# Kernel tuning notes

Measured on AMD Instinct MI355X. Metric: run time of the kernel, lower is better.

Reference implementation:

```python
import jax, jax.numpy as jnp
import numpy as np

SEQ_LEN, BATCH, TAGS = 512, 1024, 32
START_IDX, END_IDX = 30, 31
NEG = -10000.0


def setup_inputs() -> dict:
    key = jax.random.key(0)
    k1, k2 = jax.random.split(key)
    feats = jax.random.normal(k1, (SEQ_LEN, BATCH, TAGS), dtype=jnp.float32)
    mask = jnp.ones((SEQ_LEN, BATCH), dtype=jnp.float32)
    # xavier-normal-ish transition, then apply START/END constraints as in reset_parameters
    transition = jax.random.normal(k2, (TAGS, TAGS), dtype=jnp.float32) * (2.0 / (TAGS + TAGS)) ** 0.5
    transition = transition.at[START_IDX, :].set(NEG)
    transition = transition.at[:, END_IDX].set(NEG)
    return {"feats": feats, "mask": mask, "transition": transition}


def reference(feats, mask, transition):
    # feats: (T, N, M), mask: (T, N), transition: (M, M)
    batch_size, tag_size = feats.shape[1], feats.shape[2]
    alpha0 = jnp.full((batch_size, tag_size), NEG, dtype=feats.dtype)
    alpha0 = alpha0.at[:, START_IDX].set(0.0)

    def step(alpha, inp):
        feat_t, mask_t = inp  # (N, M), (N,)
        # score[n, j, i] = alpha[n, i] + transition[j, i] + feat[n, j]
        score = alpha[:, None, :] + transition[None, :, :] + feat_t[:, :, None]
        new_alpha = jax.nn.logsumexp(score, axis=-1)  # (N, M)
        m = mask_t[:, None]
        alpha = new_alpha * m + alpha * (1.0 - m)
        return alpha, None

    alpha, _ = jax.lax.scan(step, alpha0, (feats, mask))
    alpha = alpha + transition[END_IDX][None, :]
    return jax.nn.logsumexp(alpha, axis=-1)  # (N,)
```

## Files before the change

### kernel.cpp

```cpp
#include <hip/hip_runtime.h>


constexpr int SEQ = 512, BATCH = 1024, TAGS = 32;
constexpr int BPB = 8;
constexpr int CH = 8;
constexpr int NCH = (SEQ / 2) / CH;
constexpr int RINGN = 2;
constexpr int SSTRIDE = BPB * TAGS;
constexpr int FSLOT = CH * SSTRIDE;
constexpr int MSLOT = CH * BPB;

#define LOG2E 1.4426950408889634f
#define LN2   0.6931471805599453f

typedef __attribute__((ext_vector_type(8))) short short8;
typedef __attribute__((ext_vector_type(4))) float float4v;
union Frag8 { unsigned u[4]; short8 v; };

__device__ __forceinline__ unsigned pk_rn(float x, float y) {
  return __builtin_amdgcn_perm(__float_as_uint(y) + 0x8000u,
                               __float_as_uint(x) + 0x8000u, 0x07060302u);
}
__device__ __forceinline__ unsigned pk_tr(float x, float y) {
  return __builtin_amdgcn_perm(__float_as_uint(y), __float_as_uint(x), 0x07060302u);
}

template <bool FWD>
__device__ __forceinline__ void produce(
    const float* __restrict__ feats, const float* __restrict__ maskp,
    float* __restrict__ FFd, float* __restrict__ MMd,
    unsigned* __restrict__ FLGd, int b0, int lane) {
  const int bl = lane >> 3;
  const int tgd = (lane & 7) * 4;
  const size_t t0off = FWD ? 0 : (size_t)(SEQ - 1) * BATCH * TAGS;
  const float* gF = feats + t0off + (size_t)(b0 + bl) * TAGS + tgd;
  const float* gM = maskp + b0 + (lane & 7) + (FWD ? 0 : (size_t)(SEQ - 1) * BATCH);
  const ptrdiff_t fstep = FWD ? (ptrdiff_t)(BATCH * TAGS) : -(ptrdiff_t)(BATCH * TAGS);
  const ptrdiff_t mstep = FWD ? (ptrdiff_t)BATCH : -(ptrdiff_t)BATCH;
  const int wd = bl * 32 + (((lane & 7) ^ (bl & 7)) << 2);

  float4v SA[CH], SB[CH];
  float mA, mB;

#define LOADC(S, MV, c)                                                       \
  { _Pragma("unroll") for (int j = 0; j < CH; ++j)                            \
      S[j] = *(const float4v*)(gF + (ptrdiff_t)(CH * (c) + j) * fstep);       \
    MV = gM[(ptrdiff_t)(CH * (c) + (lane >> 3)) * mstep]; }

#define PROC(S, MV, c)                                                        \
  { float* fb = FFd + ((c) & (RINGN - 1)) * FSLOT;                            \
    float* mb = MMd + ((c) & (RINGN - 1)) * MSLOT;                            \
    const unsigned flag = (__ballot(MV != 0.0f) == ~0ull) ? 1u : 0u;          \
    _Pragma("unroll") for (int j = 0; j < CH; ++j) {                          \
      float4v e;                                                              \
      _Pragma("unroll") for (int i = 0; i < 4; ++i)                           \
        e[i] = __builtin_amdgcn_exp2f(S[j][i] * LOG2E);                       \
      *(float4v*)(fb + j * SSTRIDE + wd) = e;                                 \
    }                                                                         \
    mb[lane] = MV;                                                            \
    if (lane == 0) FLGd[(c) & (RINGN - 1)] = flag; }

  LOADC(SA, mA, 0)
  LOADC(SB, mB, 1)
  PROC(SA, mA, 0)
  asm volatile("s_waitcnt lgkmcnt(0)" ::: "memory");
  __builtin_amdgcn_s_barrier();
#pragma unroll 2
  for (int k = 0; k < NCH; ++k) {
    if ((k & 1) == 0) {
      if (k + 2 < NCH) LOADC(SA, mA, k + 2)
      if (k + 1 < NCH) PROC(SB, mB, k + 1)
    } else {
      if (k + 2 < NCH) LOADC(SB, mB, k + 2)
      if (k + 1 < NCH) PROC(SA, mA, k + 1)
    }
    asm volatile("s_waitcnt lgkmcnt(0)" ::: "memory");
    __builtin_amdgcn_s_barrier();
  }
  __syncthreads();
#undef LOADC
#undef PROC
}

template <bool FWD>
__device__ __forceinline__ void consume(
    const float* __restrict__ trans, float* __restrict__ out,
    const float* __restrict__ FFd, const float* __restrict__ MMd,
    const unsigned* __restrict__ FLGd,
    float* __restrict__ vbuf, float* __restrict__ c2buf, int b0, int lane) {
  const int s = lane & 15, q = lane >> 4;

  int sig[8];
#pragma unroll
  for (int i = 0; i < 8; ++i) sig[i] = (i < 4) ? (4 * q + i) : (16 + 4 * q + (i - 4));
  Frag8 e0, e1;
#pragma unroll
  for (int p = 0; p < 4; ++p) {
    if (FWD) {
      e0.u[p] = pk_rn(__builtin_amdgcn_exp2f(trans[s * TAGS + sig[2 * p]] * LOG2E),
                      __builtin_amdgcn_exp2f(trans[s * TAGS + sig[2 * p + 1]] * LOG2E));
      e1.u[p] = pk_rn(__builtin_amdgcn_exp2f(trans[(16 + s) * TAGS + sig[2 * p]] * LOG2E),
                      __builtin_amdgcn_exp2f(trans[(16 + s) * TAGS + sig[2 * p + 1]] * LOG2E));
    } else {
      e0.u[p] = pk_rn(__builtin_amdgcn_exp2f(trans[sig[2 * p] * TAGS + s] * LOG2E),
                      __builtin_amdgcn_exp2f(trans[sig[2 * p + 1] * TAGS + s] * LOG2E));
      e1.u[p] = pk_rn(__builtin_amdgcn_exp2f(trans[sig[2 * p] * TAGS + 16 + s] * LOG2E),
                      __builtin_amdgcn_exp2f(trans[sig[2 * p + 1] * TAGS + 16 + s] * LOG2E));
    }
  }

  float a[8];
#pragma unroll
  for (int i = 0; i < 8; ++i) {
    if (FWD) a[i] = (q == 3 && i == 6) ? 1.0f : 0.0f;
    else a[i] = __builtin_amdgcn_exp2f(
        trans[31 * TAGS + ((i < 4) ? (4 * q + i) : (16 + 4 * q + (i - 4)))] * LOG2E);
  }
  Frag8 Bf;
  Bf.u[0] = pk_tr(a[0], a[1]); Bf.u[1] = pk_tr(a[2], a[3]);
  Bf.u[2] = pk_tr(a[4], a[5]); Bf.u[3] = pk_tr(a[6], a[7]);
  float c2 = 0.f;
  const float4v zerov = {0.f, 0.f, 0.f, 0.f};

  const int off0 = s * 32 + ((q ^ (s & 7)) << 2);
  const int off1 = s * 32 + (((q + 4) ^ (s & 7)) << 2);

  float4v rA0, rA1, rB0, rB1;

  __builtin_amdgcn_s_barrier();
  __builtin_amdgcn_sched_barrier(0);
  rA0 = *(const float4v*)(FFd + 0 * SSTRIDE + off0);
  rA1 = *(const float4v*)(FFd + 0 * SSTRIDE + off1);
  rB0 = *(const float4v*)(FFd + 1 * SSTRIDE + off0);
  rB1 = *(const float4v*)(FFd + 1 * SSTRIDE + off1);

#define RENORM_A()                                                            \
  { float mx = fmaxf(fmaxf(fmaxf(a[0], a[1]), fmaxf(a[2], a[3])),             \
                     fmaxf(fmaxf(a[4], a[5]), fmaxf(a[6], a[7])));            \
    mx = fmaxf(mx, __shfl_xor(mx, 16, 64));                                   \
    mx = fmaxf(mx, __shfl_xor(mx, 32, 64));                                   \
    const int ex = (int)((__float_as_uint(mx) >> 23) & 0xFFu) - 127;          \
    const float scl = __uint_as_float((unsigned)(127 - ex) << 23);            \
    _Pragma("unroll") for (int i = 0; i < 8; ++i) a[i] *= scl;                \
    c2 += (float)ex; }

  for (int k = 0; k < NCH; ++k) {
    const float* fb = FFd + (k & (RINGN - 1)) * FSLOT;
    const float* mb = MMd + (k & (RINGN - 1)) * MSLOT;
    const unsigned fl = __builtin_amdgcn_readfirstlane(FLGd[k & (RINGN - 1)]);
    if (fl) {
#pragma unroll
      for (int j = 0; j < CH; ++j) {
        const float4v F0 = (j & 1) ? rB0 : rA0;
        const float4v F1 = (j & 1) ? rB1 : rA1;
        if (FWD) {
          const float4v D0 = __builtin_amdgcn_mfma_f32_16x16x32_bf16(e0.v, Bf.v, zerov, 0, 0, 0);
          const float4v D1 = __builtin_amdgcn_mfma_f32_16x16x32_bf16(e1.v, Bf.v, zerov, 0, 0, 0);
#pragma unroll
          for (int i = 0; i < 4; ++i) { a[i] = D0[i] * F0[i]; a[4 + i] = D1[i] * F1[i]; }
          if (j == CH - 1) RENORM_A()
          Bf.u[0] = pk_tr(a[0], a[1]); Bf.u[1] = pk_tr(a[2], a[3]);
          Bf.u[2] = pk_tr(a[4], a[5]); Bf.u[3] = pk_tr(a[6], a[7]);
        } else {
          float tb[8];
#pragma unroll
          for (int i = 0; i < 4; ++i) { tb[i] = a[i] * F0[i]; tb[4 + i] = a[4 + i] * F1[i]; }
          Frag8 Bp;
          Bp.u[0] = pk_tr(tb[0], tb[1]); Bp.u[1] = pk_tr(tb[2], tb[3]);
          Bp.u[2] = pk_tr(tb[4], tb[5]); Bp.u[3] = pk_tr(tb[6], tb[7]);
          const float4v D0 = __builtin_amdgcn_mfma_f32_16x16x32_bf16(e0.v, Bp.v, zerov, 0, 0, 0);
          const float4v D1 = __builtin_amdgcn_mfma_f32_16x16x32_bf16(e1.v, Bp.v, zerov, 0, 0, 0);
#pragma unroll
          for (int i = 0; i < 4; ++i) { a[i] = D0[i]; a[4 + i] = D1[i]; }
          if (j == CH - 1) RENORM_A()
        }
        if (j < CH - 2) {
          ((j & 1) ? rB0 : rA0) = *(const float4v*)(fb + (j + 2) * SSTRIDE + off0);
          ((j & 1) ? rB1 : rA1) = *(const float4v*)(fb + (j + 2) * SSTRIDE + off1);
        }
      }
    } else {
#pragma unroll
      for (int j = 0; j < CH; ++j) {
        const float4v F0 = (j & 1) ? rB0 : rA0;
        const float4v F1 = (j & 1) ? rB1 : rA1;
        const bool mv = (mb[j * BPB + (s & 7)] != 0.0f);
        if (FWD) {
          const float4v D0 = __builtin_amdgcn_mfma_f32_16x16x32_bf16(e0.v, Bf.v, zerov, 0, 0, 0);
          const float4v D1 = __builtin_amdgcn_mfma_f32_16x16x32_bf16(e1.v, Bf.v, zerov, 0, 0, 0);
#pragma unroll
          for (int i = 0; i < 4; ++i) {
            a[i] = mv ? D0[i] * F0[i] : a[i];
            a[4 + i] = mv ? D1[i] * F1[i] : a[4 + i];
          }
          if (j == CH - 1) RENORM_A()
          Bf.u[0] = pk_tr(a[0], a[1]); Bf.u[1] = pk_tr(a[2], a[3]);
          Bf.u[2] = pk_tr(a[4], a[5]); Bf.u[3] = pk_tr(a[6], a[7]);
        } else {
          float tb[8];
#pragma unroll
          for (int i = 0; i < 4; ++i) { tb[i] = a[i] * F0[i]; tb[4 + i] = a[4 + i] * F1[i]; }
          Frag8 Bp;
          Bp.u[0] = pk_tr(tb[0], tb[1]); Bp.u[1] = pk_tr(tb[2], tb[3]);
          Bp.u[2] = pk_tr(tb[4], tb[5]); Bp.u[3] = pk_tr(tb[6], tb[7]);
          const float4v D0 = __builtin_amdgcn_mfma_f32_16x16x32_bf16(e0.v, Bp.v, zerov, 0, 0, 0);
          const float4v D1 = __builtin_amdgcn_mfma_f32_16x16x32_bf16(e1.v, Bp.v, zerov, 0, 0, 0);
#pragma unroll
          for (int i = 0; i < 4; ++i) {
            a[i] = mv ? D0[i] : a[i];
            a[4 + i] = mv ? D1[i] : a[4 + i];
          }
          if (j == CH - 1) RENORM_A()
        }
        if (j < CH - 2) {
          ((j & 1) ? rB0 : rA0) = *(const float4v*)(fb + (j + 2) * SSTRIDE + off0);
          ((j & 1) ? rB1 : rA1) = *(const float4v*)(fb + (j + 2) * SSTRIDE + off1);
        }
      }
    }
    asm volatile("s_waitcnt lgkmcnt(0)" ::: "memory");
    __builtin_amdgcn_s_barrier();
    __builtin_amdgcn_sched_barrier(0);
    if (k < NCH - 1) {
      const float* fn = FFd + ((k + 1) & (RINGN - 1)) * FSLOT;
      rA0 = *(const float4v*)(fn + 0 * SSTRIDE + off0);
      rA1 = *(const float4v*)(fn + 0 * SSTRIDE + off1);
      rB0 = *(const float4v*)(fn + 1 * SSTRIDE + off0);
      rB1 = *(const float4v*)(fn + 1 * SSTRIDE + off1);
    }
  }
#undef RENORM_A

  if (!FWD) {
    float4v lo = {a[0], a[1], a[2], a[3]}, hi = {a[4], a[5], a[6], a[7]};
    *(float4v*)(vbuf + lane * 8) = lo;
    *(float4v*)(vbuf + lane * 8 + 4) = hi;
    if (lane < 8) c2buf[lane] = c2;
  }
  __syncthreads();
  if (FWD) {
    const float4v v0 = *(const float4v*)(vbuf + lane * 8);
    const float4v v1 = *(const float4v*)(vbuf + lane * 8 + 4);
    float dot = a[0] * v0[0] + a[1] * v0[1] + a[2] * v0[2] + a[3] * v0[3] +
                a[4] * v1[0] + a[5] * v1[1] + a[6] * v1[2] + a[7] * v1[3];
    dot += __shfl_xor(dot, 16, 64);
    dot += __shfl_xor(dot, 32, 64);
    if (lane < 8)
      out[b0 + lane] = LN2 * (c2 + c2buf[lane] + __builtin_amdgcn_logf(dot));
  }
}

extern "C" __global__ void __launch_bounds__(256, 1) crf_scan(
    const float* __restrict__ feats, const float* __restrict__ mask,
    const float* __restrict__ trans, float* __restrict__ out) {
  __shared__ float FF[2][RINGN][FSLOT];
  __shared__ float MM[2][RINGN][MSLOT];
  __shared__ unsigned FLG[2][RINGN];
  __shared__ float vbuf[512];
  __shared__ float c2buf[16];
  const int wid = threadIdx.x >> 6;
  const int lane = threadIdx.x & 63;
  const int b0 = blockIdx.x * BPB;

  if (wid == 0)
    consume<true>(trans, out, &FF[0][0][0], &MM[0][0][0], &FLG[0][0], vbuf, c2buf, b0, lane);
  else if (wid == 1)
    consume<false>(trans, out, &FF[1][0][0], &MM[1][0][0], &FLG[1][0], vbuf, c2buf, b0, lane);
  else if (wid == 2)
    produce<true>(feats, mask, &FF[0][0][0], &MM[0][0][0], &FLG[0][0], b0, lane);
  else
    produce<false>(feats, mask, &FF[1][0][0], &MM[1][0][0], &FLG[1][0], b0, lane);
}

extern "C" void kernel_launch(void* const* d_in, const int* in_sizes, int n_in,
                              void* d_out, int out_size, void* d_ws, size_t ws_size,
                              hipStream_t stream) {
  const float* feats = (const float*)d_in[0];
  const float* mask  = (const float*)d_in[1];
  const float* trans = (const float*)d_in[2];
  float* out = (float*)d_out;
  hipLaunchKernelGGL(crf_scan, dim3(BATCH / BPB), dim3(256), 0, stream,
                     feats, mask, trans, out);
}
```

Measured before the change: 106.9 us.

## Stream feats into LDS via async global_load_lds with four-deep raw ring

The producer wave now issues direct global-to-LDS loads into a four-slot raw ring instead of loading the chunks into registers. A separate transform pass reads the raw LDS data, applies exp2, and writes the double-buffered tile the consumer reads. This deepens the prefetch to four chunks ahead without register pressure, aiming to hide global memory latency in the serial scan. In exchange it uses more LDS, adds an extra LDS read per element, and depends on hand-counted vmcnt waits being correct.

```diff
diff --git a/kernel.cpp b/kernel.cpp
--- a/kernel.cpp
+++ b/kernel.cpp
@@ -5,9 +5,10 @@
 constexpr int BPB = 8;
 constexpr int CH = 8;
 constexpr int NCH = (SEQ / 2) / CH;
-constexpr int RINGN = 2;
+constexpr int RRN = 4;
 constexpr int SSTRIDE = BPB * TAGS;
 constexpr int FSLOT = CH * SSTRIDE;
+constexpr int RSLOT = FSLOT + 64;
 constexpr int MSLOT = CH * BPB;
 
 #define LOG2E 1.4426950408889634f
@@ -25,61 +26,76 @@
   return __builtin_amdgcn_perm(__float_as_uint(y), __float_as_uint(x), 0x07060302u);
 }
 
+__device__ __forceinline__ void gld16(const float* g, float* l) {
+  __builtin_amdgcn_global_load_lds((const __attribute__((address_space(1))) void*)g,
+                                   (__attribute__((address_space(3))) void*)l, 16, 0, 0);
+}
+__device__ __forceinline__ void gld4(const float* g, float* l) {
+  __builtin_amdgcn_global_load_lds((const __attribute__((address_space(1))) void*)g,
+                                   (__attribute__((address_space(3))) void*)l, 4, 0, 0);
+}
+
 template <bool FWD>
 __device__ __forceinline__ void produce(
     const float* __restrict__ feats, const float* __restrict__ maskp,
-    float* __restrict__ FFd, float* __restrict__ MMd,
+    float* __restrict__ RAWd, float* __restrict__ FFd, float* __restrict__ MMd,
     unsigned* __restrict__ FLGd, int b0, int lane) {
-  const int bl = lane >> 3;
-  const int tgd = (lane & 7) * 4;
+  const int bs = lane >> 3;
+  const int tg = 4 * ((lane & 7) ^ (bs & 7));
   const size_t t0off = FWD ? 0 : (size_t)(SEQ - 1) * BATCH * TAGS;
-  const float* gF = feats + t0off + (size_t)(b0 + bl) * TAGS + tgd;
-  const float* gM = maskp + b0 + (lane & 7) + (FWD ? 0 : (size_t)(SEQ - 1) * BATCH);
+  const float* gF0 = feats + t0off + (size_t)(b0 + bs) * TAGS + tg;
+  const float* gM0 = maskp +
+      (FWD ? (size_t)(lane >> 3) : (size_t)(SEQ - 1 - (lane >> 3))) * BATCH +
+      b0 + (lane & 7);
   const ptrdiff_t fstep = FWD ? (ptrdiff_t)(BATCH * TAGS) : -(ptrdiff_t)(BATCH * TAGS);
   const ptrdiff_t mstep = FWD ? (ptrdiff_t)BATCH : -(ptrdiff_t)BATCH;
-  const int wd = bl * 32 + (((lane & 7) ^ (bl & 7)) << 2);
-
-  float4v SA[CH], SB[CH];
-  float mA, mB;
-
-#define LOADC(S, MV, c)                                                       \
-  { _Pragma("unroll") for (int j = 0; j < CH; ++j)                            \
-      S[j] = *(const float4v*)(gF + (ptrdiff_t)(CH * (c) + j) * fstep);       \
-    MV = gM[(ptrdiff_t)(CH * (c) + (lane >> 3)) * mstep]; }
-
-#define PROC(S, MV, c)                                                        \
-  { float* fb = FFd + ((c) & (RINGN - 1)) * FSLOT;                            \
-    float* mb = MMd + ((c) & (RINGN - 1)) * MSLOT;                            \
-    const unsigned flag = (__ballot(MV != 0.0f) == ~0ull) ? 1u : 0u;          \
-    _Pragma("unroll") for (int j = 0; j < CH; ++j) {                          \
-      float4v e;                                                              \
-      _Pragma("unroll") for (int i = 0; i < 4; ++i)                           \
-        e[i] = __builtin_amdgcn_exp2f(S[j][i] * LOG2E);                       \
-      *(float4v*)(fb + j * SSTRIDE + wd) = e;                                 \
-    }                                                                         \
-    mb[lane] = MV;                                                            \
-    if (lane == 0) FLGd[(c) & (RINGN - 1)] = flag; }
-
-  LOADC(SA, mA, 0)
-  LOADC(SB, mB, 1)
-  PROC(SA, mA, 0)
+
+  auto FILL = [&](int k) {
+    float* rb = RAWd + (k & (RRN - 1)) * RSLOT;
+#pragma unroll
+    for (int j = 0; j < CH; ++j)
+      gld16(gF0 + (ptrdiff_t)(CH * k + j) * fstep, rb + j * SSTRIDE);
+    gld4(gM0 + (ptrdiff_t)(CH * k) * mstep, rb + FSLOT);
+  };
+
+  auto XFORM = [&](int c) {
+    const float* rb = RAWd + (c & (RRN - 1)) * RSLOT;
+    float* fb = FFd + (c & 1) * FSLOT;
+    const float mraw = rb[FSLOT + lane];
+    const unsigned flag = (__ballot(mraw != 0.0f) == ~0ull) ? 1u : 0u;
+#pragma unroll
+    for (int j = 0; j < CH; ++j) {
+      const float4v r = *(const float4v*)(rb + j * SSTRIDE + lane * 4);
+      float4v e;
+#pragma unroll
+      for (int i = 0; i < 4; ++i) e[i] = __builtin_amdgcn_exp2f(r[i] * LOG2E);
+      *(float4v*)(fb + j * SSTRIDE + lane * 4) = e;
+    }
+    MMd[(c & 1) * MSLOT + lane] = mraw;
+    if (lane == 0) FLGd[c & 1] = flag;
+  };
+
+  FILL(0); FILL(1); FILL(2); FILL(3);
+  asm volatile("s_waitcnt vmcnt(27)" ::: "memory");
+  XFORM(0);
   asm volatile("s_waitcnt lgkmcnt(0)" ::: "memory");
   __builtin_amdgcn_s_barrier();
-#pragma unroll 2
   for (int k = 0; k < NCH; ++k) {
-    if ((k & 1) == 0) {
-      if (k + 2 < NCH) LOADC(SA, mA, k + 2)
-      if (k + 1 < NCH) PROC(SB, mB, k + 1)
-    } else {
-      if (k + 2 < NCH) LOADC(SB, mB, k + 2)
-      if (k + 1 < NCH) PROC(SA, mA, k + 1)
-    }
+    if (k < NCH - 4) {
+      FILL(k + 4);
+      asm volatile("s_waitcnt vmcnt(27)" ::: "memory");
+    } else if (k == NCH - 4) {
+      asm volatile("s_waitcnt vmcnt(18)" ::: "memory");
+    } else if (k == NCH - 3) {
+      asm volatile("s_waitcnt vmcnt(9)" ::: "memory");
+    } else if (k == NCH - 2) {
+      asm volatile("s_waitcnt vmcnt(0)" ::: "memory");
+    }
+    if (k + 1 < NCH) XFORM(k + 1);
     asm volatile("s_waitcnt lgkmcnt(0)" ::: "memory");
     __builtin_amdgcn_s_barrier();
   }
   __syncthreads();
-#undef LOADC
-#undef PROC
 }
 
 template <bool FWD>
@@ -145,9 +161,9 @@
     c2 += (float)ex; }
 
   for (int k = 0; k < NCH; ++k) {
-    const float* fb = FFd + (k & (RINGN - 1)) * FSLOT;
-    const float* mb = MMd + (k & (RINGN - 1)) * MSLOT;
-    const unsigned fl = __builtin_amdgcn_readfirstlane(FLGd[k & (RINGN - 1)]);
+    const float* fb = FFd + (k & 1) * FSLOT;
+    const float* mb = MMd + (k & 1) * MSLOT;
+    const unsigned fl = __builtin_amdgcn_readfirstlane(FLGd[k & 1]);
     if (fl) {
 #pragma unroll
       for (int j = 0; j < CH; ++j) {
@@ -222,7 +238,7 @@
     __builtin_amdgcn_s_barrier();
     __builtin_amdgcn_sched_barrier(0);
     if (k < NCH - 1) {
-      const float* fn = FFd + ((k + 1) & (RINGN - 1)) * FSLOT;
+      const float* fn = FFd + ((k + 1) & 1) * FSLOT;
       rA0 = *(const float4v*)(fn + 0 * SSTRIDE + off0);
       rA1 = *(const float4v*)(fn + 0 * SSTRIDE + off1);
       rB0 = *(const float4v*)(fn + 1 * SSTRIDE + off0);
@@ -253,9 +269,10 @@
 extern "C" __global__ void __launch_bounds__(256, 1) crf_scan(
     const float* __restrict__ feats, const float* __restrict__ mask,
     const float* __restrict__ trans, float* __restrict__ out) {
-  __shared__ float FF[2][RINGN][FSLOT];
-  __shared__ float MM[2][RINGN][MSLOT];
-  __shared__ unsigned FLG[2][RINGN];
+  __shared__ float FF[2][2][FSLOT];
+  __shared__ float MM[2][2][MSLOT];
+  __shared__ unsigned FLG[2][2];
+  __shared__ float RAW[2][RRN][RSLOT];
   __shared__ float vbuf[512];
   __shared__ float c2buf[16];
   const int wid = threadIdx.x >> 6;
@@ -267,9 +284,9 @@
   else if (wid == 1)
     consume<false>(trans, out, &FF[1][0][0], &MM[1][0][0], &FLG[1][0], vbuf, c2buf, b0, lane);
   else if (wid == 2)
-    produce<true>(feats, mask, &FF[0][0][0], &MM[0][0][0], &FLG[0][0], b0, lane);
+    produce<true>(feats, mask, &RAW[0][0][0], &FF[0][0][0], &MM[0][0][0], &FLG[0][0], b0, lane);
   else
-    produce<false>(feats, mask, &FF[1][0][0], &MM[1][0][0], &FLG[1][0], b0, lane);
+    produce<false>(feats, mask, &RAW[1][0][0], &FF[1][0][0], &MM[1][0][0], &FLG[1][0], b0, lane);
 }
 
 extern "C" void kernel_launch(void* const* d_in, const int* in_sizes, int n_in,
```

After: 115.3 us. 7.8% more time.
